# Optimization experiments

Measured on AMD Instinct MI355X. Metric: run time of the kernel, lower is better.

Reference implementation:

```python
import jax, jax.numpy as jnp
import numpy as np
from jax import lax

B, C, H, W = 8, 256, 64, 64
HEADS = 8
STRIDE = 2


def _grouped_conv(x, w, b, stride, groups):
    # x: [B, Cin, H, W]; w: [Cout, Cin/groups, k, k] (OIHW)
    y = lax.conv_general_dilated(x, w, (stride, stride), 'VALID',
                                 dimension_numbers=('NCHW', 'OIHW', 'NCHW'),
                                 feature_group_count=groups)
    return y + b[None, :, None, None]


def _grouped_conv_transpose(x, w, b, stride, groups):
    # Equivalent of torch ConvTranspose2d(kernel=stride, stride=stride, groups=groups)
    # implemented as lhs-dilated conv. w: [Cout, Cin/groups, k, k] (already in conv-equivalent layout).
    k = w.shape[-1]
    pad = k - 1
    y = lax.conv_general_dilated(x, w, (1, 1), [(pad, pad), (pad, pad)],
                                 lhs_dilation=(stride, stride),
                                 dimension_numbers=('NCHW', 'OIHW', 'NCHW'),
                                 feature_group_count=groups)
    return y + b[None, :, None, None]


def setup_inputs() -> dict:
    key = jax.random.key(0)
    ks = jax.random.split(key, 12)
    s = 0.05
    inp = {
        'q': jax.random.normal(ks[0], (B, C, H, W), jnp.float32),
        'k': jax.random.normal(ks[1], (B, C, H, W), jnp.float32),
        'v': jax.random.normal(ks[2], (B, C, H, W), jnp.float32),
        # grouped QKV conv weights: groups=C, out=C*HEADS -> [C*HEADS, 1, s, s]
        'wq': jax.random.normal(ks[3], (C * HEADS, 1, STRIDE, STRIDE), jnp.float32) * s,
        'bq': jax.random.normal(ks[4], (C * HEADS,), jnp.float32) * s,
        'wk': jax.random.normal(ks[5], (C * HEADS, 1, STRIDE, STRIDE), jnp.float32) * s,
        'bk': jax.random.normal(ks[6], (C * HEADS,), jnp.float32) * s,
        'wv': jax.random.normal(ks[7], (C * HEADS, 1, STRIDE, STRIDE), jnp.float32) * s,
        'bv': jax.random.normal(ks[8], (C * HEADS,), jnp.float32) * s,
        # deconv (groups=C, in=C*HEADS, out=C) in conv-equivalent OIHW layout: [C, HEADS, s, s]
        'wo': jax.random.normal(ks[9], (C, HEADS, STRIDE, STRIDE), jnp.float32) * s,
        'bo': jax.random.normal(ks[10], (C,), jnp.float32) * s,
        'gamma': jax.random.normal(ks[11], (1,), jnp.float32),
    }
    return inp


def reference(q, k, v, wq, bq, wk, bk, wv, bv, wo, bo, gamma):
    Bn, Cq, Hq, Wsp = q.shape
    Ckv = k.shape[1]
    # grouped conv projections -> [B, heads, C, L]
    pq = _grouped_conv(q, wq, bq, STRIDE, Cq).reshape(Bn, HEADS, Cq, -1)
    pk = _grouped_conv(k, wk, bk, STRIDE, Ckv).reshape(Bn, HEADS, Ckv, -1)
    pv = _grouped_conv(v, wv, bv, STRIDE, Ckv).reshape(Bn, HEADS, Ckv, -1)
    scale = pq.shape[3] ** (-0.5)
    # channel-wise attention: [B, h, Cq, Ckv]
    attn = jax.nn.softmax(jnp.einsum('bhcl,bhdl->bhcd', pq, pk) * scale, axis=-1)
    out = jnp.einsum('bhcd,bhdl->bhcl', attn, pv)  # [B, h, Cq, L]
    out = out.reshape(Bn, HEADS * Cq, Hq // STRIDE, Wsp // STRIDE)
    out = _grouped_conv_transpose(out, wo, bo, STRIDE, Cq)  # [B, Cq, Hq, Wsp]
    # dropout is identity at inference
    return q + out * gamma
```

## Files before the change

kernel.cpp:

```cpp
#include <hip/hip_runtime.h>
#include <hip/hip_bf16.h>

typedef __bf16 bf16;
typedef __bf16 bf16x4 __attribute__((ext_vector_type(4)));
typedef __bf16 bf16x8 __attribute__((ext_vector_type(8)));
typedef float f32x4 __attribute__((ext_vector_type(4)));
typedef long i64;

__device__ __forceinline__ void gload16(const void* g, void* l) {
  __builtin_amdgcn_global_load_lds(
      (const __attribute__((address_space(1))) unsigned int*)g,
      (__attribute__((address_space(3))) unsigned int*)l, 16, 0, 0);
}


__global__ __launch_bounds__(256) void proj_kqv(
    const float* __restrict__ kin, const float* __restrict__ qin,
    const float* __restrict__ vin,
    const float* __restrict__ wk, const float* __restrict__ bk,
    const float* __restrict__ wq, const float* __restrict__ bq,
    const float* __restrict__ wv, const float* __restrict__ bv,
    char* __restrict__ Pk, char* __restrict__ Pq, char* __restrict__ Vt) {
  int b = blockIdx.y;
  int x = blockIdx.x;
  int t = threadIdx.x;
  __shared__ __attribute__((aligned(16))) char smem[17152];
  if (x < 256) {
    bool isq = x >= 128;
    int g0 = (x & 127)*2;
    const float* in   = isq ? qin : kin;
    const float* w    = isq ? wq : wk;
    const float* bias = isq ? bq : bk;
    char* out         = isq ? Pq : Pk;
    int ch = t >> 7, kb = (t >> 3) & 15, gcol = t & 7;
    int g = g0 + ch;
    float4 wj[8]; float bj[8];
#pragma unroll
    for (int j = 0; j < 8; j++) {
      wj[j] = reinterpret_cast<const float4*>(w)[g*8 + j];
      bj[j] = bias[g*8 + j];
    }
    const char* chg = (const char*)(in + ((size_t)b*256 + g)*4096);
    int m = kb*2 + (gcol >> 2);
    int cb = (gcol & 3)*64;
    const float4* R0 = reinterpret_cast<const float4*>(chg + (2*m)*256 + cb);
    const float4* R1 = reinterpret_cast<const float4*>(chg + (2*m+1)*256 + cb);
    float f0[16], f1[16];
#pragma unroll
    for (int u = 0; u < 4; u++) {
      *reinterpret_cast<float4*>(f0 + u*4) = R0[u];
      *reinterpret_cast<float4*>(f1 + u*4) = R1[u];
    }
    int bh = b*8 + (g >> 5);
    int c0l = (g & 31)*8;
    char* rowbase = out + (((size_t)bh*16 + kb)*256 + c0l)*64;
#pragma unroll
    for (int j = 0; j < 8; j++) {
      float ov[8];
#pragma unroll
      for (int u = 0; u < 8; u++)
        ov[u] = bj[j] + wj[j].x*f0[2*u] + wj[j].y*f0[2*u+1] + wj[j].z*f1[2*u] + wj[j].w*f1[2*u+1];
      int w0 = 0, w1 = 0;
      w0 = __builtin_amdgcn_cvt_pk_fp8_f32(ov[0], ov[1], w0, false);
      w0 = __builtin_amdgcn_cvt_pk_fp8_f32(ov[2], ov[3], w0, true);
      w1 = __builtin_amdgcn_cvt_pk_fp8_f32(ov[4], ov[5], w1, false);
      w1 = __builtin_amdgcn_cvt_pk_fp8_f32(ov[6], ov[7], w1, true);
      int2 st; st.x = w0; st.y = w1;
      *reinterpret_cast<int2*>(rowbase + j*64 + ((gcol ^ j)*8)) = st;
    }
  } else {
    float* ch = reinterpret_cast<float*>(smem);
    int r = x - 256;
    int m = r & 31, h = r >> 5;
    {
      int seg = t >> 2, part = t & 3;
      int gl = seg >> 1, ky = seg & 1;
      const float* src = vin + (((size_t)b*256 + h*32 + gl)*64 + (2*m + ky))*64;
      float* drow = ch + (gl*2 + ky)*67;
#pragma unroll
      for (int i = 0; i < 4; i++) {
        float4 v = reinterpret_cast<const float4*>(src)[part + i*4];
        int x0 = (part + i*4)*4;
        drow[x0]=v.x; drow[x0+1]=v.y; drow[x0+2]=v.z; drow[x0+3]=v.w;
      }
    }
    int cgrp = t & 31, lgr = t >> 5;
    int c0 = cgrp*8;
    float4 wv8[8]; float bb8[8];
#pragma unroll
    for (int u = 0; u < 8; u++) {
      wv8[u] = reinterpret_cast<const float4*>(wv)[h*256 + c0 + u];
      bb8[u] = bv[h*256 + c0 + u];
    }
    __syncthreads();
    const float* r0 = ch + (cgrp*2 + 0)*67;
    const float* r1 = ch + (cgrp*2 + 1)*67;
    int bh = b*8 + h;
    char* base = Vt + ((size_t)bh*4 + (c0 >> 6))*65536;
    int gsw = ((cgrp & 7) ^ lgr)*8;
#pragma unroll
    for (int p = 0; p < 4; p++) {
      int n = p*8 + lgr;
      int l = m*32 + n;
      float c00 = r0[2*n], c01 = r0[2*n+1], c10 = r1[2*n], c11 = r1[2*n+1];
      float ov[8];
#pragma unroll
      for (int u = 0; u < 8; u++)
        ov[u] = 8.f*(bb8[u] + wv8[u].x*c00 + wv8[u].y*c01 + wv8[u].z*c10 + wv8[u].w*c11);
      int w0 = 0, w1 = 0;
      w0 = __builtin_amdgcn_cvt_pk_fp8_f32(ov[0], ov[1], w0, false);
      w0 = __builtin_amdgcn_cvt_pk_fp8_f32(ov[2], ov[3], w0, true);
      w1 = __builtin_amdgcn_cvt_pk_fp8_f32(ov[4], ov[5], w1, false);
      w1 = __builtin_amdgcn_cvt_pk_fp8_f32(ov[6], ov[7], w1, true);
      int2 st; st.x = w0; st.y = w1;
      *reinterpret_cast<int2*>(base + (size_t)l*64 + gsw) = st;
    }
  }
}

__global__ __launch_bounds__(256, 2) void attn_qk(
    const char* __restrict__ Pq, const char* __restrict__ Pk,
    char* __restrict__ Pattn) {
  int raw = blockIdx.x;
  int idx = raw >> 3;
  int bh = (raw & 7)*8 + (idx >> 2);
  int cs = idx & 3;
  int t = threadIdx.x, wave = t >> 6, lane = t & 63, lg = lane >> 4, lr = lane & 15;
  __shared__ __attribute__((aligned(16))) char smem[40960];
  char* Kb0 = smem;
  char* Kb1 = smem + 16384;
  char* Qb0 = smem + 32768;
  char* Qb1 = smem + 36864;
  float (*red)[64] = reinterpret_cast<float (*)[64]>(smem + 32768);
  char* Pst = smem;
  const char* Kbase = Pk + (size_t)bh*262144 + wave*4096 + lane*16;
  const char* Qbase = Pq + (size_t)bh*262144 + (size_t)cs*4096 + wave*1024 + lane*16;
  char* Kd0 = Kb0 + wave*4096;  char* Kd1 = Kb1 + wave*4096;
  char* Qd0 = Qb0 + wave*1024;  char* Qd1 = Qb1 + wave*1024;

#define STAGE(kb, K_, Q_) { \
    const char* kc = Kbase + (size_t)(kb)*16384; \
    _Pragma("unroll") \
    for (int i_ = 0; i_ < 4; i_++) gload16(kc + i_*1024, (K_) + i_*1024); \
    gload16(Qbase + (size_t)(kb)*16384, (Q_)); }

  f32x4 acc[4][4];
#pragma unroll
  for (int i = 0; i < 4; i++)
#pragma unroll
    for (int j = 0; j < 4; j++) { f32x4 z = {0.f,0.f,0.f,0.f}; acc[i][j] = z; }

  STAGE(0, Kd0, Qd0);
#pragma unroll
  for (int kb = 0; kb < 16; kb++) {
    if (kb < 15) {
      if (kb & 1) { STAGE(kb+1, Kd0, Qd0); } else { STAGE(kb+1, Kd1, Qd1); }
      asm volatile("s_waitcnt vmcnt(5)" ::: "memory");
    } else {
      asm volatile("s_waitcnt vmcnt(0)" ::: "memory");
    }
    __builtin_amdgcn_s_barrier();
    __builtin_amdgcn_sched_barrier(0);
    const char* Kc = (kb & 1) ? Kb1 : Kb0;
    const char* Qc = (kb & 1) ? Qb1 : Qb0;
#pragma unroll
    for (int ks = 0; ks < 2; ks++) {
      int colx = (ks*32 + lg*8) ^ ((lr & 7) << 3);
      i64 a[4];
#pragma unroll
      for (int mi = 0; mi < 4; mi++)
        a[mi] = *reinterpret_cast<const i64*>(Qc + (mi*16 + lr)*64 + colx);
#pragma unroll
      for (int ni = 0; ni < 4; ni++) {
        i64 bfr = *reinterpret_cast<const i64*>(Kc + (wave*64 + ni*16 + lr)*64 + colx);
#pragma unroll
        for (int mi = 0; mi < 4; mi++)
          acc[mi][ni] = __builtin_amdgcn_mfma_f32_16x16x32_fp8_fp8(a[mi], bfr, acc[mi][ni], 0, 0, 0);
      }
    }
    __builtin_amdgcn_s_barrier();
    __builtin_amdgcn_sched_barrier(0);
  }
#undef STAGE
  const float scale = 0.03125f;
  float sums[4][4];
#pragma unroll
  for (int mi = 0; mi < 4; mi++)
#pragma unroll
    for (int r = 0; r < 4; r++) {
      float mx = fmaxf(fmaxf(acc[mi][0][r], acc[mi][1][r]), fmaxf(acc[mi][2][r], acc[mi][3][r]));
#pragma unroll
      for (int off = 1; off < 16; off <<= 1) mx = fmaxf(mx, __shfl_xor(mx, off, 64));
      red[wave][mi*16 + lg*4 + r] = mx;
    }
  __syncthreads();
#pragma unroll
  for (int mi = 0; mi < 4; mi++)
#pragma unroll
    for (int r = 0; r < 4; r++) {
      int clr = mi*16 + lg*4 + r;
      float mx = fmaxf(fmaxf(red[0][clr], red[1][clr]), fmaxf(red[2][clr], red[3][clr]));
      float s = 0.f;
#pragma unroll
      for (int ni = 0; ni < 4; ni++) {
        float p = __expf(scale*(acc[mi][ni][r] - mx));
        acc[mi][ni][r] = p; s += p;
      }
#pragma unroll
      for (int off = 1; off < 16; off <<= 1) s += __shfl_xor(s, off, 64);
      sums[mi][r] = s;
    }
  __syncthreads();
#pragma unroll
  for (int mi = 0; mi < 4; mi++)
#pragma unroll
    for (int r = 0; r < 4; r++) red[wave][mi*16 + lg*4 + r] = sums[mi][r];
  __syncthreads();
#pragma unroll
  for (int mi = 0; mi < 4; mi++)
#pragma unroll
    for (int r = 0; r < 4; r++) {
      int clr = mi*16 + lg*4 + r;
      float iv = 32.f/(red[0][clr] + red[1][clr] + red[2][clr] + red[3][clr]);
      char* prow = Pst + wave*4096 + clr*64;
      int xr = (clr & 7) << 3;
#pragma unroll
      for (int ni = 0; ni < 4; ni += 2) {
        int pk2 = __builtin_amdgcn_cvt_pk_fp8_f32(acc[mi][ni][r]*iv, acc[mi][ni+1][r]*iv, 0, false);
        prow[(ni*16 + lr) ^ xr]     = (char)(pk2 & 0xff);
        prow[((ni+1)*16 + lr) ^ xr] = (char)((pk2 >> 8) & 0xff);
      }
    }
  __syncthreads();
  const uint4* ls = reinterpret_cast<const uint4*>(Pst);
#pragma unroll
  for (int i = 0; i < 4; i++) {
    int f = i*256 + t;
    int kb = f >> 8, rem = f & 255;
    char* dst = Pattn + ((size_t)(bh*4 + kb)*256 + cs*64)*64 + (size_t)rem*16;
    *reinterpret_cast<uint4*>(dst) = ls[f];
  }
}

__global__ __launch_bounds__(256, 4) void pv_deconv(const char* __restrict__ Pattn,
    const char* __restrict__ Vt, const float* __restrict__ qin,
    const float* __restrict__ wo, const float* __restrict__ bo,
    const float* __restrict__ gamma, float* __restrict__ outp) {
  int raw = blockIdx.x;
  int idx = raw >> 3;
  int pair = (raw & 7)*32 + (idx >> 2);
  int tb = idx & 3;
  int mb = pair & 3, bh = pair >> 2;
  int h = bh & 7, b = bh >> 3;
  int t = threadIdx.x, wave = t >> 6, lane = t & 63, lg = lane >> 4, lr = lane & 15;
  __shared__ __attribute__((aligned(16))) char smem[40960];
  char* Pl   = smem;
  char* Vl   = smem + 4096;
  bf16* OlT  = reinterpret_cast<bf16*>(smem);
  float* wo_s = reinterpret_cast<float*>(smem + 36864);
  float* bo_s = reinterpret_cast<float*>(smem + 37888);
  const char* Pbase = Pattn + (size_t)bh*65536 + tb*4096;
  const char* Vbase = Vt + (size_t)bh*262144 + mb*16384;
  f32x4 acc[4][4];
#pragma unroll
  for (int i = 0; i < 4; i++)
#pragma unroll
    for (int j = 0; j < 4; j++) { f32x4 z = {0.f,0.f,0.f,0.f}; acc[i][j] = z; }
  for (int kb = 0; kb < 4; kb++) {
    __syncthreads();
    {
      const char* pc = Pbase + (size_t)kb*16384 + wave*1024 + lane*16;
      gload16(pc, Pl + wave*1024);
      const char* vc = Vbase + (size_t)kb*65536 + wave*4096 + lane*16;
      char* vl = Vl + wave*4096;
#pragma unroll
      for (int i = 0; i < 4; i++) gload16(vc + i*1024, vl + i*1024);
    }
    __syncthreads();
#pragma unroll
    for (int ks = 0; ks < 2; ks++) {
      int colx = (ks*32 + lg*8) ^ ((lr & 7) << 3);
      i64 a[4];
#pragma unroll
      for (int mi = 0; mi < 4; mi++)
        a[mi] = *reinterpret_cast<const i64*>(Pl + (mi*16 + lr)*64 + colx);
#pragma unroll
      for (int ni = 0; ni < 4; ni++) {
        i64 bfr = *reinterpret_cast<const i64*>(Vl + (wave*64 + ni*16 + lr)*64 + colx);
#pragma unroll
        for (int mi = 0; mi < 4; mi++)
          acc[mi][ni] = __builtin_amdgcn_mfma_f32_16x16x32_fp8_fp8(a[mi], bfr, acc[mi][ni], 0, 0, 0);
      }
    }
  }
  __syncthreads();
  const float rescale = 1.f/256.f;
#pragma unroll
  for (int mi = 0; mi < 4; mi++)
#pragma unroll
    for (int ni = 0; ni < 4; ni++) {
      int l = wave*64 + ni*16 + lr;
      int cb = mi*16 + lg*4;
      bf16x4 p;
      p[0] = (bf16)(acc[mi][ni][0]*rescale); p[1] = (bf16)(acc[mi][ni][1]*rescale);
      p[2] = (bf16)(acc[mi][ni][2]*rescale); p[3] = (bf16)(acc[mi][ni][3]*rescale);
      *reinterpret_cast<bf16x4*>(OlT + l*66 + cb) = p;
    }
  wo_s[t] = wo[((size_t)(h*32 + tb*8 + (t>>5)))*32 + (t & 31)];
  if (t < 8) bo_s[t] = bo[h*32 + tb*8 + t];
  __syncthreads();
  int xq = t & 15, b5 = (t >> 4) & 1, ct = t >> 5;
  float2 wp[8];
#pragma unroll
  for (int j = 0; j < 8; j++)
    wp[j] = *reinterpret_cast<const float2*>(wo_s + ct*32 + j*4 + (1 - b5)*2);
  float bias = bo_s[ct];
  float gm = gamma[0];
  int co = h*32 + tb*8 + ct;
#pragma unroll
  for (int it = 0; it < 8; it++) {
    int y = it*2 + b5;
    int ll0 = it*32 + xq*2;
    bf16x4 o00 = *reinterpret_cast<const bf16x4*>(OlT + ll0*66 + ct*8);
    bf16x4 o01 = *reinterpret_cast<const bf16x4*>(OlT + ll0*66 + ct*8 + 4);
    bf16x4 o10 = *reinterpret_cast<const bf16x4*>(OlT + (ll0+1)*66 + ct*8);
    bf16x4 o11 = *reinterpret_cast<const bf16x4*>(OlT + (ll0+1)*66 + ct*8 + 4);
    float v0 = bias, v1 = bias, v2 = bias, v3 = bias;
#pragma unroll
    for (int j = 0; j < 4; j++) {
      float f0 = (float)o00[j], f1 = (float)o01[j];
      v0 += f0*wp[j].y;   v1 += f0*wp[j].x;
      v0 += f1*wp[4+j].y; v1 += f1*wp[4+j].x;
      float g0 = (float)o10[j], g1 = (float)o11[j];
      v2 += g0*wp[j].y;   v3 += g0*wp[j].x;
      v2 += g1*wp[4+j].y; v3 += g1*wp[4+j].x;
    }
    size_t oi = (((size_t)b*256 + co)*64 + (mb*16 + y))*64 + xq*4;
    float4 qv = *reinterpret_cast<const float4*>(qin + oi);
    float4 ov;
    ov.x = qv.x + gm*v0; ov.y = qv.y + gm*v1;
    ov.z = qv.z + gm*v2; ov.w = qv.w + gm*v3;
    *reinterpret_cast<float4*>(outp + oi) = ov;
  }
}

extern "C" void kernel_launch(void* const* d_in, const int* in_sizes, int n_in,
                              void* d_out, int out_size, void* d_ws, size_t ws_size,
                              hipStream_t stream) {
  const float* q  = (const float*)d_in[0];
  const float* k  = (const float*)d_in[1];
  const float* v  = (const float*)d_in[2];
  const float* wq = (const float*)d_in[3];
  const float* bq = (const float*)d_in[4];
  const float* wk = (const float*)d_in[5];
  const float* bk = (const float*)d_in[6];
  const float* wv = (const float*)d_in[7];
  const float* bv = (const float*)d_in[8];
  const float* wo = (const float*)d_in[9];
  const float* bo = (const float*)d_in[10];
  const float* gamma = (const float*)d_in[11];
  float* out = (float*)d_out;

  char* ws = (char*)d_ws;
  char* Pk    = ws;
  char* Pq    = ws + 16777216;
  char* Vt    = ws + 33554432;
  char* Pattn = ws + 50331648;

  proj_kqv<<<dim3(512, 8), 256, 0, stream>>>(k, q, v, wk, bk, wq, bq, wv, bv, Pk, Pq, Vt);
  attn_qk <<<dim3(256), 256, 0, stream>>>(Pq, Pk, Pattn);
  pv_deconv<<<dim3(1024), 256, 0, stream>>>(Pattn, Vt, q, wo, bo, gamma, out);
}
```

Before: 69.70 us.

## Process four batches per projection block with software-pipelined loads

```diff
diff --git a/kernel.cpp b/kernel.cpp
--- a/kernel.cpp
+++ b/kernel.cpp
@@ -21,7 +21,7 @@
     const float* __restrict__ wq, const float* __restrict__ bq,
     const float* __restrict__ wv, const float* __restrict__ bv,
     char* __restrict__ Pk, char* __restrict__ Pq, char* __restrict__ Vt) {
-  int b = blockIdx.y;
+  int y = blockIdx.y;
   int x = blockIdx.x;
   int t = threadIdx.x;
   __shared__ __attribute__((aligned(16))) char smem[17152];
@@ -40,50 +40,66 @@
       wj[j] = reinterpret_cast<const float4*>(w)[g*8 + j];
       bj[j] = bias[g*8 + j];
     }
-    const char* chg = (const char*)(in + ((size_t)b*256 + g)*4096);
+    __builtin_amdgcn_sched_barrier(0);
     int m = kb*2 + (gcol >> 2);
     int cb = (gcol & 3)*64;
-    const float4* R0 = reinterpret_cast<const float4*>(chg + (2*m)*256 + cb);
-    const float4* R1 = reinterpret_cast<const float4*>(chg + (2*m+1)*256 + cb);
-    float f0[16], f1[16];
-#pragma unroll
-    for (int u = 0; u < 4; u++) {
-      *reinterpret_cast<float4*>(f0 + u*4) = R0[u];
-      *reinterpret_cast<float4*>(f1 + u*4) = R1[u];
-    }
-    int bh = b*8 + (g >> 5);
     int c0l = (g & 31)*8;
-    char* rowbase = out + (((size_t)bh*16 + kb)*256 + c0l)*64;
-#pragma unroll
-    for (int j = 0; j < 8; j++) {
-      float ov[8];
-#pragma unroll
-      for (int u = 0; u < 8; u++)
-        ov[u] = bj[j] + wj[j].x*f0[2*u] + wj[j].y*f0[2*u+1] + wj[j].z*f1[2*u] + wj[j].w*f1[2*u+1];
-      int w0 = 0, w1 = 0;
-      w0 = __builtin_amdgcn_cvt_pk_fp8_f32(ov[0], ov[1], w0, false);
-      w0 = __builtin_amdgcn_cvt_pk_fp8_f32(ov[2], ov[3], w0, true);
-      w1 = __builtin_amdgcn_cvt_pk_fp8_f32(ov[4], ov[5], w1, false);
-      w1 = __builtin_amdgcn_cvt_pk_fp8_f32(ov[6], ov[7], w1, true);
-      int2 st; st.x = w0; st.y = w1;
-      *reinterpret_cast<int2*>(rowbase + j*64 + ((gcol ^ j)*8)) = st;
-    }
+    int hh = g >> 5;
+    const char* src0 = (const char*)(in + ((size_t)(y*4)*256 + g)*4096) + (2*m)*256 + cb;
+    float fa0[16], fa1[16], fb0[16], fb1[16];
+
+#define LOADB(bb, F0, F1) { \
+    const char* s_ = src0 + (size_t)(bb)*4194304; \
+    const float4* R0 = reinterpret_cast<const float4*>(s_); \
+    const float4* R1 = reinterpret_cast<const float4*>(s_ + 256); \
+    _Pragma("unroll") \
+    for (int u = 0; u < 4; u++) { \
+      *reinterpret_cast<float4*>((F0) + u*4) = R0[u]; \
+      *reinterpret_cast<float4*>((F1) + u*4) = R1[u]; \
+    } }
+
+#define CONVB(bb, F0, F1) { \
+    int bh = (y*4 + (bb))*8 + hh; \
+    char* rowbase = out + (((size_t)bh*16 + kb)*256 + c0l)*64; \
+    _Pragma("unroll") \
+    for (int j = 0; j < 8; j++) { \
+      float ov[8]; \
+      _Pragma("unroll") \
+      for (int u = 0; u < 8; u++) \
+        ov[u] = bj[j] + wj[j].x*(F0)[2*u] + wj[j].y*(F0)[2*u+1] + wj[j].z*(F1)[2*u] + wj[j].w*(F1)[2*u+1]; \
+      int w0 = 0, w1 = 0; \
+      w0 = __builtin_amdgcn_cvt_pk_fp8_f32(ov[0], ov[1], w0, false); \
+      w0 = __builtin_amdgcn_cvt_pk_fp8_f32(ov[2], ov[3], w0, true); \
+      w1 = __builtin_amdgcn_cvt_pk_fp8_f32(ov[4], ov[5], w1, false); \
+      w1 = __builtin_amdgcn_cvt_pk_fp8_f32(ov[6], ov[7], w1, true); \
+      int2 st; st.x = w0; st.y = w1; \
+      *reinterpret_cast<int2*>(rowbase + j*64 + ((gcol ^ j)*8)) = st; \
+    } }
+
+    LOADB(0, fa0, fa1);
+    LOADB(1, fb0, fb1);
+    __builtin_amdgcn_sched_barrier(0);
+    asm volatile("s_waitcnt vmcnt(8)" ::: "memory");
+    CONVB(0, fa0, fa1);
+    __builtin_amdgcn_sched_barrier(0);
+    LOADB(2, fa0, fa1);
+    __builtin_amdgcn_sched_barrier(0);
+    asm volatile("s_waitcnt vmcnt(16)" ::: "memory");
+    CONVB(1, fb0, fb1);
+    __builtin_amdgcn_sched_barrier(0);
+    LOADB(3, fb0, fb1);
+    __builtin_amdgcn_sched_barrier(0);
+    asm volatile("s_waitcnt vmcnt(16)" ::: "memory");
+    CONVB(2, fa0, fa1);
+    __builtin_amdgcn_sched_barrier(0);
+    asm volatile("s_waitcnt vmcnt(8)" ::: "memory");
+    CONVB(3, fb0, fb1);
+#undef LOADB
+#undef CONVB
   } else {
     float* ch = reinterpret_cast<float*>(smem);
     int r = x - 256;
     int m = r & 31, h = r >> 5;
-    {
-      int seg = t >> 2, part = t & 3;
-      int gl = seg >> 1, ky = seg & 1;
-      const float* src = vin + (((size_t)b*256 + h*32 + gl)*64 + (2*m + ky))*64;
-      float* drow = ch + (gl*2 + ky)*67;
-#pragma unroll
-      for (int i = 0; i < 4; i++) {
-        float4 v = reinterpret_cast<const float4*>(src)[part + i*4];
-        int x0 = (part + i*4)*4;
-        drow[x0]=v.x; drow[x0+1]=v.y; drow[x0+2]=v.z; drow[x0+3]=v.w;
-      }
-    }
     int cgrp = t & 31, lgr = t >> 5;
     int c0 = cgrp*8;
     float4 wv8[8]; float bb8[8];
@@ -92,28 +108,45 @@
       wv8[u] = reinterpret_cast<const float4*>(wv)[h*256 + c0 + u];
       bb8[u] = bv[h*256 + c0 + u];
     }
-    __syncthreads();
+    int seg = t >> 2, part = t & 3;
+    int gl = seg >> 1, ky = seg & 1;
+    const float* src00 = vin + (((size_t)(y*4)*256 + h*32 + gl)*64 + (2*m + ky))*64;
+    float* drow = ch + (gl*2 + ky)*67;
     const float* r0 = ch + (cgrp*2 + 0)*67;
     const float* r1 = ch + (cgrp*2 + 1)*67;
-    int bh = b*8 + h;
-    char* base = Vt + ((size_t)bh*4 + (c0 >> 6))*65536;
     int gsw = ((cgrp & 7) ^ lgr)*8;
-#pragma unroll
-    for (int p = 0; p < 4; p++) {
-      int n = p*8 + lgr;
-      int l = m*32 + n;
-      float c00 = r0[2*n], c01 = r0[2*n+1], c10 = r1[2*n], c11 = r1[2*n+1];
-      float ov[8];
-#pragma unroll
-      for (int u = 0; u < 8; u++)
-        ov[u] = 8.f*(bb8[u] + wv8[u].x*c00 + wv8[u].y*c01 + wv8[u].z*c10 + wv8[u].w*c11);
-      int w0 = 0, w1 = 0;
-      w0 = __builtin_amdgcn_cvt_pk_fp8_f32(ov[0], ov[1], w0, false);
-      w0 = __builtin_amdgcn_cvt_pk_fp8_f32(ov[2], ov[3], w0, true);
-      w1 = __builtin_amdgcn_cvt_pk_fp8_f32(ov[4], ov[5], w1, false);
-      w1 = __builtin_amdgcn_cvt_pk_fp8_f32(ov[6], ov[7], w1, true);
-      int2 st; st.x = w0; st.y = w1;
-      *reinterpret_cast<int2*>(base + (size_t)l*64 + gsw) = st;
+    for (int bb = 0; bb < 4; bb++) {
+      int b = y*4 + bb;
+      __syncthreads();
+      {
+        const float* src = src00 + (size_t)bb*1048576;
+#pragma unroll
+        for (int i = 0; i < 4; i++) {
+          float4 v = reinterpret_cast<const float4*>(src)[part + i*4];
+          int x0 = (part + i*4)*4;
+          drow[x0]=v.x; drow[x0+1]=v.y; drow[x0+2]=v.z; drow[x0+3]=v.w;
+        }
+      }
+      __syncthreads();
+      int bh = b*8 + h;
+      char* base = Vt + ((size_t)bh*4 + (c0 >> 6))*65536;
+#pragma unroll
+      for (int p = 0; p < 4; p++) {
+        int n = p*8 + lgr;
+        int l = m*32 + n;
+        float c00 = r0[2*n], c01 = r0[2*n+1], c10 = r1[2*n], c11 = r1[2*n+1];
+        float ov[8];
+#pragma unroll
+        for (int u = 0; u < 8; u++)
+          ov[u] = 8.f*(bb8[u] + wv8[u].x*c00 + wv8[u].y*c01 + wv8[u].z*c10 + wv8[u].w*c11);
+        int w0 = 0, w1 = 0;
+        w0 = __builtin_amdgcn_cvt_pk_fp8_f32(ov[0], ov[1], w0, false);
+        w0 = __builtin_amdgcn_cvt_pk_fp8_f32(ov[2], ov[3], w0, true);
+        w1 = __builtin_amdgcn_cvt_pk_fp8_f32(ov[4], ov[5], w1, false);
+        w1 = __builtin_amdgcn_cvt_pk_fp8_f32(ov[6], ov[7], w1, true);
+        int2 st; st.x = w0; st.y = w1;
+        *reinterpret_cast<int2*>(base + (size_t)l*64 + gsw) = st;
+      }
     }
   }
 }
@@ -367,7 +400,7 @@
   char* Vt    = ws + 33554432;
   char* Pattn = ws + 50331648;
 
-  proj_kqv<<<dim3(512, 8), 256, 0, stream>>>(k, q, v, wk, bk, wq, bq, wv, bv, Pk, Pq, Vt);
+  proj_kqv<<<dim3(512, 2), 256, 0, stream>>>(k, q, v, wk, bk, wq, bq, wv, bv, Pk, Pq, Vt);
   attn_qk <<<dim3(256), 256, 0, stream>>>(Pq, Pk, Pattn);
   pv_deconv<<<dim3(1024), 256, 0, stream>>>(Pattn, Vt, q, wo, bo, gamma, out);
 }
```

Measured after the change: 69.86 us. About the same (+0.2%).
